# Kernel optimization log

Hardware: AMD Instinct MI355X
Metric: run time of the kernel (lower is better)

Reference implementation:

```python
import jax, jax.numpy as jnp
import numpy as np

HEADS = 8
DIM_HEAD = 64
NH = 16
NW = 16
SCALE = DIM_HEAD ** -0.5


def _avg2x2(a):
    # 2x2 average pool, stride 1, over axes 1,2 of [B,H,W,C] (== unfold+mean in torch)
    return (a[:, :-1, :-1] + a[:, 1:, :-1] + a[:, :-1, 1:] + a[:, 1:, 1:]) * 0.25


def _split_heads(t):
    B, n, _ = t.shape
    return t.reshape(B, n, HEADS, DIM_HEAD).transpose(0, 2, 1, 3)  # b h n d


def setup_inputs() -> dict:
    key = jax.random.key(0)
    ks = jax.random.split(key, 5)
    B, n, dim = 64, 482, 512
    inner = HEADS * DIM_HEAD
    return {
        "x": jax.random.normal(ks[0], (B, n, dim), jnp.float32),
        "mask": jax.random.normal(ks[1], (B, n, dim), jnp.float32),
        "W_qkv": jax.random.normal(ks[2], (3 * inner, dim), jnp.float32) * 0.02,
        "W_out": jax.random.normal(ks[3], (dim, inner), jnp.float32) * 0.02,
        "b_out": jax.random.normal(ks[4], (dim,), jnp.float32) * 0.02,
    }


def reference(x, mask, W_qkv, W_out, b_out):
    sg = jax.lax.stop_gradient
    B, n, dim = x.shape
    inner = HEADS * DIM_HEAD
    nHW = NH * NW            # 256
    nb = (NH - 1) * (NW - 1)  # 225

    # qkv projection
    qkv = x @ W_qkv.T                              # [B,n,3*inner]
    q, k, v = (
        _split_heads(t) for t in jnp.split(qkv, 3, axis=-1)
    )

    # mask path (no grad)
    mask_ = sg(mask)
    updated = (jnp.mean(mask_[:, 1:], axis=-1, keepdims=True) > 0.0).astype(x.dtype)
    updated = jnp.concatenate([jnp.ones_like(updated[:, :1]), updated], axis=1)  # [B,n,1]
    qkv_m = mask_ @ jnp.abs(sg(W_qkv)).T
    q_m, k_m, v_m = (_split_heads(t) for t in jnp.split(qkv_m, 3, axis=-1))
    q_m = q_m / (1e-6 + jnp.max(q_m, axis=2, keepdims=True))
    k_m = k_m / (1e-6 + jnp.max(k_m, axis=2, keepdims=True))
    v_m = v_m / (1e-6 + jnp.max(v_m, axis=2, keepdims=True))
    q_m, k_m, v_m = sg(q_m), sg(k_m), sg(v_m)

    # mask-modulated attention
    dots = jnp.einsum('bhnd,bhmd->bhnm', q * q_m, k * k_m) * SCALE
    attn = jax.nn.softmax(dots, axis=-1)
    out = jnp.einsum('bhnm,bhmd->bhnd', attn, v_m * v)
    out = out.transpose(0, 2, 1, 3).reshape(B, n, inner) * updated

    m = jnp.einsum('bhnm,bhmd->bhnd', sg(attn), v_m)
    m = sg(m.transpose(0, 2, 1, 3).reshape(B, n, inner) * updated)

    # overlap blending (is_overlap=True)
    inv_tail = 1.0 - updated[:, -nb:]
    inv_grid = 1.0 - updated[:, 1:nHW + 1]

    out_bridge = _avg2x2(out[:, 1:nHW + 1].reshape(B, NH, NW, inner)).reshape(B, nb, inner) * inv_tail
    out_origin = jnp.pad(out[:, -nb:].reshape(B, NH - 1, NW - 1, inner),
                         ((0, 0), (1, 1), (1, 1), (0, 0)))
    out_origin = _avg2x2(out_origin).reshape(B, nHW, inner) * inv_grid

    m_bridge = _avg2x2(m[:, 1:nHW + 1].reshape(B, NH, NW, inner)).reshape(B, nb, inner) * inv_tail
    m_origin = jnp.pad(m[:, -nb:].reshape(B, NH - 1, NW - 1, inner),
                       ((0, 0), (1, 1), (1, 1), (0, 0)))
    m_origin = _avg2x2(m_origin).reshape(B, nHW, inner) * inv_grid

    out = out.at[:, 1:nHW + 1].add(out_origin).at[:, -nb:].add(out_bridge)
    m = sg(m.at[:, 1:nHW + 1].add(m_origin).at[:, -nb:].add(m_bridge))

    # nearest-neighbor interpolation of mask means (no grad)
    mm = jnp.mean(m[:, 1:], axis=-1, keepdims=True)          # [B,n-1,1]
    a = mm[:, :nHW].reshape(B, 1, NH, NW)
    inter = jnp.repeat(jnp.repeat(a, 16, axis=2), 16, axis=3)  # [B,1,256,256]
    b = mm[:, -nb:].reshape(B, 1, NH - 1, NW - 1)
    inter_shift = jnp.repeat(jnp.repeat(b, 16, axis=2), 16, axis=3)  # [B,1,240,240]
    inter = inter.at[:, :, 8:-8, 8:-8].set((inter[:, :, 8:-8, 8:-8] + inter_shift) * 0.5)
    inter = sg(inter)

    m = sg(m @ jnp.abs(sg(W_out)).T)

    out_final = out @ W_out.T + b_out
    return out_final, m, inter
```

## Files before the change

### kernel.cpp

```cpp
#include <hip/hip_runtime.h>

#define B_      64
#define NSEQ    482
#define DIM     512
#define HEADS_  8
#define HD      64
#define QKV3    1536
#define NPAD    512
#define MROWS   (B_ * NSEQ)
#define GT      4096

typedef __bf16 v8bf __attribute__((ext_vector_type(8)));
typedef float  v4f  __attribute__((ext_vector_type(4)));
typedef unsigned int v4u __attribute__((ext_vector_type(4)));

typedef __attribute__((address_space(1))) const unsigned short gu16;
typedef __attribute__((address_space(3))) unsigned short lu16;

__device__ __forceinline__ unsigned short f2bf(float f) {
    unsigned u = __float_as_uint(f);
    u += 0x7fffu + ((u >> 16) & 1u);
    return (unsigned short)(u >> 16);
}
__device__ __forceinline__ float bf2f(unsigned short h) {
    return __uint_as_float(((unsigned)h) << 16);
}
__device__ __forceinline__ v8bf vabs8(v8bf x) {
    v4u u;
    __builtin_memcpy(&u, &x, 16);
    u &= (v4u){0x7fff7fffu, 0x7fff7fffu, 0x7fff7fffu, 0x7fff7fffu};
    v8bf r;
    __builtin_memcpy(&r, &u, 16);
    return r;
}

__global__ void k_cvt(const float* __restrict__ s, unsigned short* __restrict__ d, int n4) {
    int i = blockIdx.x * 256 + threadIdx.x;
    if (i < n4) {
        float4 v = ((const float4*)s)[i];
        ushort4 o;
        o.x = f2bf(v.x); o.y = f2bf(v.y); o.z = f2bf(v.z); o.w = f2bf(v.w);
        ((ushort4*)d)[i] = o;
    }
}

__global__ __launch_bounds__(256) void k_cvtmask(const float* __restrict__ mask,
                                                 unsigned short* __restrict__ mb,
                                                 float* __restrict__ upd) {
    int row = blockIdx.x * 4 + (threadIdx.x >> 6);
    int lane = threadIdx.x & 63;
    const float4* p = (const float4*)(mask + (size_t)row * DIM);
    ushort4* d = (ushort4*)(mb + (size_t)row * DIM);
    float s = 0.f;
    #pragma unroll
    for (int j = 0; j < 2; j++) {
        float4 v = p[j * 64 + lane];
        ushort4 o;
        o.x = f2bf(v.x); o.y = f2bf(v.y); o.z = f2bf(v.z); o.w = f2bf(v.w);
        d[j * 64 + lane] = o;
        s += v.x + v.y + v.z + v.w;
    }
    #pragma unroll
    for (int off = 32; off; off >>= 1) s += __shfl_xor(s, off);
    if (lane == 0) {
        int i = row % NSEQ;
        upd[row] = (i == 0) ? 1.f : ((s > 0.f) ? 1.f : 0.f);
    }
}

__global__ __launch_bounds__(512, 4) void k_gemm2(const unsigned short* __restrict__ A1,
                                                  const unsigned short* __restrict__ A2,
                                                  const unsigned short* __restrict__ Bw,
                                                  unsigned short* __restrict__ C1b,
                                                  unsigned short* __restrict__ C2b,
                                                  float* __restrict__ C1f,
                                                  float* __restrict__ C2f,
                                                  const float* __restrict__ bias,
                                                  int N, int K) {
    __shared__ __align__(16) unsigned short As1[3 * GT];
    __shared__ __align__(16) unsigned short As2[3 * GT];
    __shared__ __align__(16) unsigned short Bs[3 * GT];
    int tid = threadIdx.x;
    int lane = tid & 63, w = tid >> 6;
    int grp = w >> 2;
    int wm = (w >> 1) & 1, wn = w & 1;
    int quad = lane >> 4, m16 = lane & 15;

    int nbx = gridDim.x, nwg = nbx * gridDim.y;
    int id = blockIdx.y * nbx + blockIdx.x;
    int q = nwg >> 3, r = nwg & 7;
    int xcd = id & 7, sub = id >> 3;
    int nid = (xcd < r ? xcd * (q + 1) : r * (q + 1) + (xcd - r) * q) + sub;
    int m0 = (nid / nbx) * 128, n0 = (nid % nbx) * 128;

    int srow = tid >> 2, scol = (tid & 3) * 8;
    const unsigned short* gA1 = &A1[(size_t)(m0 + srow) * K + scol];
    const unsigned short* gA2 = &A2[(size_t)(m0 + srow) * K + scol];
    const unsigned short* gB  = &Bw[(size_t)(n0 + srow) * K + scol];
    lu16* lA1 = (lu16*)&As1[w * 512];
    lu16* lA2 = (lu16*)&As2[w * 512];
    lu16* lB  = (lu16*)&Bs[w * 512];

    v4f acc[4][4];
    #pragma unroll
    for (int i = 0; i < 4; i++)
        #pragma unroll
        for (int j = 0; j < 4; j++) acc[i][j] = (v4f){0.f, 0.f, 0.f, 0.f};

    auto STAGE = [&](int bo, int s) {
        int ko = s << 5;
        __builtin_amdgcn_global_load_lds((gu16*)(gA1 + ko), lA1 + bo, 16, 0, 0);
        __builtin_amdgcn_global_load_lds((gu16*)(gA2 + ko), lA2 + bo, 16, 0, 0);
        __builtin_amdgcn_global_load_lds((gu16*)(gB  + ko), lB  + bo, 16, 0, 0);
    };
    const unsigned short* Ams = grp ? As2 : As1;
    auto COMPUTE = [&](int bo) {
        v8bf a[4];
        #pragma unroll
        for (int i = 0; i < 4; i++)
            a[i] = *(const v8bf*)&Ams[bo + (wm * 64 + i * 16 + m16) * 32 + quad * 8];
        #pragma unroll
        for (int j = 0; j < 4; j++) {
            v8bf b = *(const v8bf*)&Bs[bo + (wn * 64 + j * 16 + m16) * 32 + quad * 8];
            if (grp) b = vabs8(b);
            #pragma unroll
            for (int i = 0; i < 4; i++)
                acc[i][j] = __builtin_amdgcn_mfma_f32_16x16x32_bf16(a[i], b, acc[i][j], 0, 0, 0);
        }
    };

    int steps = K >> 5;
    STAGE(0, 0);
    STAGE(GT, 1);
    int b0 = 0, b1 = GT, b2 = 2 * GT;
    for (int s = 0; s < steps; ++s) {
        if (s < steps - 1) asm volatile("s_waitcnt vmcnt(3)" ::: "memory");
        else               asm volatile("s_waitcnt vmcnt(0)" ::: "memory");
        __builtin_amdgcn_s_barrier();
        __builtin_amdgcn_sched_barrier(0);
        if (s + 2 < steps) STAGE(b2, s + 2);
        COMPUTE(b0);
        int t = b0; b0 = b1; b1 = b2; b2 = t;
    }
    __syncthreads();

    if (C1f) {
        float* Cf = grp ? C2f : C1f;
        #pragma unroll
        for (int j = 0; j < 4; j++) {
            int col = n0 + wn * 64 + j * 16 + m16;
            float bi = (bias && !grp) ? bias[col] : 0.f;
            #pragma unroll
            for (int i = 0; i < 4; i++) {
                int rowb = m0 + wm * 64 + i * 16 + quad * 4;
                #pragma unroll
                for (int r = 0; r < 4; r++) {
                    size_t off = (size_t)(rowb + r) * N + col;
                    Cf[off] = acc[i][j][r] + bi;
                }
            }
        }
    } else {
        unsigned short* Cb = grp ? C2b : C1b;
        unsigned short* wbuf = &As1[w * 1024];
        int rr = lane >> 2;
        int c0 = ((lane & 3) * 2) ^ ((rr >> 1) & 7);
        size_t colb = n0 + wn * 64 + (lane & 3) * 16;
        #pragma unroll
        for (int i = 0; i < 4; i++) {
            #pragma unroll
            for (int j = 0; j < 4; j++)
                #pragma unroll
                for (int r = 0; r < 4; r++) {
                    int row = quad * 4 + r;
                    int e = j * 16 + m16;
                    int es = ((((e >> 3) ^ ((row >> 1) & 7)) << 3) | (e & 7));
                    wbuf[row * 64 + es] = f2bf(acc[i][j][r]);
                }
            int4 p0 = *(const int4*)&wbuf[rr * 64 + c0 * 8];
            int4 p1 = *(const int4*)&wbuf[rr * 64 + (c0 ^ 1) * 8];
            size_t off0 = (size_t)(m0 + wm * 64 + i * 16 + rr) * N + colb;
            *(int4*)&Cb[off0] = p0;
            *(int4*)&Cb[off0 + 8] = p1;
        }
    }
}

__global__ void k_colmax(const unsigned short* __restrict__ qm, float* __restrict__ invsc) {
    int b = blockIdx.x;
    int c = blockIdx.y * 256 + threadIdx.x;
    const unsigned short* p = qm + (size_t)b * NSEQ * QKV3 + c;
    float mx = -1e30f;
    for (int i = 0; i < NSEQ; i++) mx = fmaxf(mx, bf2f(p[(size_t)i * QKV3]));
    invsc[b * QKV3 + c] = 1.f / (1e-6f + mx);
}

__global__ __launch_bounds__(256) void k_build(const unsigned short* __restrict__ qkv,
                                               const unsigned short* __restrict__ qm,
                                               const float* __restrict__ invsc,
                                               unsigned short* __restrict__ QQ,
                                               unsigned short* __restrict__ KK,
                                               unsigned short* __restrict__ VVt,
                                               unsigned short* __restrict__ VMt) {
    __shared__ unsigned short tv[64][72];
    __shared__ unsigned short tm[64][72];
    int tid = threadIdx.x;
    int dd = tid & 63, il = tid >> 6;
    int it = blockIdx.x, h = blockIdx.y, b = blockIdx.z;
    int i0 = it * 64;
    size_t bh = (size_t)(b * HEADS_ + h);
    int c = h * HD + dd;
    float invq = invsc[b * QKV3 + c] * 0.125f;
    float invk = invsc[b * QKV3 + 512 + c];
    float invv = invsc[b * QKV3 + 1024 + c];
    #pragma unroll 4
    for (int p = 0; p < 16; p++) {
        int li = p * 4 + il;
        int i = i0 + li;
        unsigned short oq = 0, ok = 0, ov = 0, om = 0;
        if (i < NSEQ) {
            size_t base = ((size_t)(b * NSEQ + i)) * QKV3 + c;
            float q  = bf2f(qkv[base]),        qv = bf2f(qm[base]);
            float kk = bf2f(qkv[base + 512]),  kv = bf2f(qm[base + 512]);
            float vv = bf2f(qkv[base + 1024]), vm = bf2f(qm[base + 1024]);
            oq = f2bf(q * qv * invq);
            ok = f2bf(kk * kv * invk);
            float vmn = vm * invv;
            ov = f2bf(vv * vmn);
            om = f2bf(vmn);
        }
        QQ[(bh * NPAD + i) * HD + dd] = oq;
        KK[(bh * NPAD + i) * HD + dd] = ok;
        tv[li][dd] = ov;
        tm[li][dd] = om;
    }
    __syncthreads();
    #pragma unroll 4
    for (int p = 0; p < 16; p++) {
        int dr = p * 4 + il;
        VVt[(bh * HD + dr) * NPAD + i0 + dd] = tv[dd][dr];
        VMt[(bh * HD + dr) * NPAD + i0 + dd] = tm[dd][dr];
    }
}

__global__ __launch_bounds__(256, 3) void k_attn(const unsigned short* __restrict__ QQ,
                                                 const unsigned short* __restrict__ KK,
                                                 const unsigned short* __restrict__ VVt,
                                                 const unsigned short* __restrict__ VMt,
                                                 const float* __restrict__ upd,
                                                 float* __restrict__ OUT1,
                                                 float* __restrict__ M1) {
    __shared__ __align__(16) unsigned short Ks[2][32 * 72];
    __shared__ __align__(16) unsigned short Vs[2][64 * 40];
    __shared__ __align__(16) unsigned short Ms[2][64 * 40];
    __shared__ __align__(16) unsigned short Ps[4][32 * 40];

    int tid = threadIdx.x;
    int w = tid >> 6, lane = tid & 63;
    int quad = lane >> 4, m16 = lane & 15;
    int id = (blockIdx.z * 8 + blockIdx.y) * 4 + blockIdx.x;
    int nid = (id & 7) * 256 + (id >> 3);
    int b = nid >> 5, h = (nid >> 2) & 7;
    int q0 = (nid & 3) * 128 + w * 32;
    size_t bh = (size_t)(b * HEADS_ + h);

    v8bf aq[2][2];
    #pragma unroll
    for (int s = 0; s < 2; s++) {
        const unsigned short* qb = &QQ[(bh * NPAD + q0 + s * 16 + m16) * HD];
        aq[s][0] = *(const v8bf*)&qb[quad * 8];
        aq[s][1] = *(const v8bf*)&qb[32 + quad * 8];
    }

    v4f vacc[2][4], macc[2][4];
    #pragma unroll
    for (int s = 0; s < 2; s++)
        #pragma unroll
        for (int dt = 0; dt < 4; dt++) {
            vacc[s][dt] = (v4f){0.f, 0.f, 0.f, 0.f};
            macc[s][dt] = (v4f){0.f, 0.f, 0.f, 0.f};
        }
    float lrun[2][4];
    #pragma unroll
    for (int s = 0; s < 2; s++)
        #pragma unroll
        for (int r = 0; r < 4; r++) lrun[s][r] = 0.f;

    const unsigned short* gK = &KK[bh * NPAD * HD + tid * 8];
    const unsigned short* gV = &VVt[(bh * HD + (tid >> 2)) * NPAD + (tid & 3) * 8];
    const unsigned short* gM = &VMt[(bh * HD + (tid >> 2)) * NPAD + (tid & 3) * 8];
    int oK = (tid >> 3) * 72 + (tid & 7) * 8;
    int oV = (tid >> 2) * 40 + (tid & 3) * 8;
    unsigned short* Pw = &Ps[w][0];

    int4 rk = *(const int4*)gK;
    int4 rv = *(const int4*)gV;
    int4 rm = *(const int4*)gM;

    for (int ic = 0; ic < 16; ++ic) {
        int buf = ic & 1;
        *(int4*)&Ks[buf][oK] = rk;
        *(int4*)&Vs[buf][oV] = rv;
        *(int4*)&Ms[buf][oV] = rm;
        if (ic < 15) {
            rk = *(const int4*)(gK + (ic + 1) * 32 * HD);
            rv = *(const int4*)(gV + (ic + 1) * 32);
            rm = *(const int4*)(gM + (ic + 1) * 32);
        }
        __syncthreads();

        v8bf kf[2][2];
        #pragma unroll
        for (int t = 0; t < 2; t++) {
            kf[t][0] = *(const v8bf*)&Ks[buf][(t * 16 + m16) * 72 + quad * 8];
            kf[t][1] = *(const v8bf*)&Ks[buf][(t * 16 + m16) * 72 + 32 + quad * 8];
        }
        v4f S[2][2];
        #pragma unroll
        for (int s = 0; s < 2; s++)
            #pragma unroll
            for (int t = 0; t < 2; t++) {
                v4f a = (v4f){0.f, 0.f, 0.f, 0.f};
                a = __builtin_amdgcn_mfma_f32_16x16x32_bf16(aq[s][0], kf[t][0], a, 0, 0, 0);
                a = __builtin_amdgcn_mfma_f32_16x16x32_bf16(aq[s][1], kf[t][1], a, 0, 0, 0);
                S[s][t] = a;
            }

        int i0 = ic * 32;
        if (i0 + 32 > NSEQ) {
            bool x0 = (i0 + m16) >= NSEQ;
            bool x1 = (i0 + 16 + m16) >= NSEQ;
            #pragma unroll
            for (int s = 0; s < 2; s++)
                #pragma unroll
                for (int r = 0; r < 4; r++) {
                    if (x0) S[s][0][r] = -1e30f;
                    if (x1) S[s][1][r] = -1e30f;
                }
        }

        #pragma unroll
        for (int s = 0; s < 2; s++)
            #pragma unroll
            for (int r = 0; r < 4; r++) {
                float e0 = __expf(S[s][0][r]);
                float e1 = __expf(S[s][1][r]);
                lrun[s][r] += e0 + e1;
                Pw[(s * 16 + quad * 4 + r) * 40 + m16] = f2bf(e0);
                Pw[(s * 16 + quad * 4 + r) * 40 + 16 + m16] = f2bf(e1);
            }

        v8bf ap[2];
        ap[0] = *(const v8bf*)&Pw[m16 * 40 + quad * 8];
        ap[1] = *(const v8bf*)&Pw[(16 + m16) * 40 + quad * 8];

        #pragma unroll
        for (int dt = 0; dt < 4; dt++) {
            v8bf bv = *(const v8bf*)&Vs[buf][(dt * 16 + m16) * 40 + quad * 8];
            v8bf bm = *(const v8bf*)&Ms[buf][(dt * 16 + m16) * 40 + quad * 8];
            #pragma unroll
            for (int s = 0; s < 2; s++) {
                vacc[s][dt] = __builtin_amdgcn_mfma_f32_16x16x32_bf16(ap[s], bv, vacc[s][dt], 0, 0, 0);
                macc[s][dt] = __builtin_amdgcn_mfma_f32_16x16x32_bf16(ap[s], bm, macc[s][dt], 0, 0, 0);
            }
        }
    }

    #pragma unroll
    for (int s = 0; s < 2; s++)
        #pragma unroll
        for (int r = 0; r < 4; r++) {
            float sum = lrun[s][r];
            sum += __shfl_xor(sum, 1);
            sum += __shfl_xor(sum, 2);
            sum += __shfl_xor(sum, 4);
            sum += __shfl_xor(sum, 8);
            float iv = 1.f / sum;
            int iq = q0 + s * 16 + quad * 4 + r;
            if (iq < NSEQ) {
                float u = upd[b * NSEQ + iq] * iv;
                size_t off = ((size_t)(b * NSEQ + iq)) * DIM + h * HD + m16;
                #pragma unroll
                for (int dt = 0; dt < 4; dt++) {
                    OUT1[off + dt * 16] = vacc[s][dt][r] * u;
                    M1[off + dt * 16]   = macc[s][dt][r] * u;
                }
            }
        }
}

__global__ __launch_bounds__(256) void k_blend(const float* __restrict__ O1,
                                               const float* __restrict__ Mm,
                                               const float* __restrict__ upd,
                                               unsigned short* __restrict__ O2,
                                               unsigned short* __restrict__ M2,
                                               float* __restrict__ mm) {
    int blk = blockIdx.x;
    int b = blk / NSEQ, i = blk - b * NSEQ;
    int tid = threadIdx.x;
    size_t rb = (size_t)blk * DIM;
    int ns = 0;
    size_t src[4];
    float wgt = 0.f;
    if (i >= 1) {
        wgt = 0.25f * (1.f - upd[blk]);
        if (wgt != 0.f) {
            if (i <= 256) {
                int g = i - 1, gy = g >> 4, gx = g & 15;
                #pragma unroll
                for (int dy = 0; dy < 2; dy++)
                    #pragma unroll
                    for (int dx = 0; dx < 2; dx++) {
                        int sy = gy - 1 + dy, sx = gx - 1 + dx;
                        if (sy >= 0 && sy < 15 && sx >= 0 && sx < 15)
                            src[ns++] = ((size_t)(b * NSEQ + 257 + sy * 15 + sx)) * DIM;
                    }
            } else {
                int t = i - 257, ty = t / 15, tx = t - ty * 15;
                #pragma unroll
                for (int dy = 0; dy < 2; dy++)
                    #pragma unroll
                    for (int dx = 0; dx < 2; dx++)
                        src[ns++] = ((size_t)(b * NSEQ + 1 + (ty + dy) * 16 + (tx + dx))) * DIM;
            }
        }
    }
    float msum = 0.f;
    for (int c = tid; c < DIM; c += 256) {
        float o = O1[rb + c], m = Mm[rb + c];
        float ao = 0.f, am = 0.f;
        for (int s = 0; s < ns; s++) { ao += O1[src[s] + c]; am += Mm[src[s] + c]; }
        o += wgt * ao;
        m += wgt * am;
        O2[rb + c] = f2bf(o);
        M2[rb + c] = f2bf(m);
        msum += m;
    }
    #pragma unroll
    for (int off = 32; off; off >>= 1) msum += __shfl_xor(msum, off);
    __shared__ float red[4];
    if ((tid & 63) == 0) red[tid >> 6] = msum;
    __syncthreads();
    if (tid == 0 && i >= 1)
        mm[b * 481 + i - 1] = (red[0] + red[1] + red[2] + red[3]) * (1.f / 512.f);
}

__global__ void k_inter(const float* __restrict__ mm, float* __restrict__ dst) {
    int idx = blockIdx.x * 256 + threadIdx.x;
    int b = idx >> 16, rem = idx & 65535;
    int y = rem >> 8, x = rem & 255;
    const float* mb = mm + b * 481;
    float v = mb[((y >> 4) << 4) + (x >> 4)];
    if (y >= 8 && y < 248 && x >= 8 && x < 248)
        v = 0.5f * (v + mb[256 + ((y - 8) >> 4) * 15 + ((x - 8) >> 4)]);
    dst[idx] = v;
}

extern "C" void kernel_launch(void* const* d_in, const int* in_sizes, int n_in,
                              void* d_out, int out_size, void* d_ws, size_t ws_size,
                              hipStream_t stream) {
    const float* x    = (const float*)d_in[0];
    const float* mask = (const float*)d_in[1];
    const float* Wqkv = (const float*)d_in[2];
    const float* Wout = (const float*)d_in[3];
    const float* bout = (const float*)d_in[4];
    float* out = (float*)d_out;

    char* ws = (char*)d_ws;
    size_t o = 0;
    auto alloc = [&](size_t bytes) -> char* {
        char* r = ws + o;
        o += (bytes + 255) & ~(size_t)255;
        return r;
    };
    unsigned short* xb    = (unsigned short*)alloc((size_t)MROWS * DIM * 2);
    unsigned short* maskb = (unsigned short*)alloc((size_t)MROWS * DIM * 2);
    unsigned short* Wb    = (unsigned short*)alloc((size_t)QKV3 * DIM * 2);
    unsigned short* Wob   = (unsigned short*)alloc((size_t)DIM * DIM * 2);
    unsigned short* qkvb  = (unsigned short*)alloc((size_t)MROWS * QKV3 * 2);
    unsigned short* qkvmb = (unsigned short*)alloc((size_t)MROWS * QKV3 * 2);
    float* upd  = (float*)alloc((size_t)MROWS * 4);
    float* invs = (float*)alloc((size_t)B_ * QKV3 * 4);
    float* mm   = (float*)alloc((size_t)B_ * 481 * 4);
    unsigned short* QQ  = (unsigned short*)alloc((size_t)B_ * HEADS_ * NPAD * HD * 2);
    unsigned short* KK  = (unsigned short*)alloc((size_t)B_ * HEADS_ * NPAD * HD * 2);
    unsigned short* VVt = (unsigned short*)alloc((size_t)B_ * HEADS_ * NPAD * HD * 2);
    unsigned short* VMt = (unsigned short*)alloc((size_t)B_ * HEADS_ * NPAD * HD * 2);
    float* OUT1 = (float*)qkvb;
    float* M1p  = (float*)qkvmb;
    unsigned short* O2 = xb;
    unsigned short* M2 = maskb;

    k_cvt<<<(MROWS * DIM / 4) / 256, 256, 0, stream>>>(x, xb, MROWS * DIM / 4);
    k_cvtmask<<<MROWS / 4, 256, 0, stream>>>(mask, maskb, upd);
    k_cvt<<<(QKV3 * DIM / 4) / 256, 256, 0, stream>>>(Wqkv, Wb, QKV3 * DIM / 4);
    k_cvt<<<(DIM * DIM / 4) / 256, 256, 0, stream>>>(Wout, Wob, DIM * DIM / 4);

    dim3 g1(QKV3 / 128, MROWS / 128);
    k_gemm2<<<g1, 512, 0, stream>>>(xb, maskb, Wb, qkvb, qkvmb,
                                    nullptr, nullptr, nullptr, QKV3, DIM);

    k_colmax<<<dim3(B_, QKV3 / 256), 256, 0, stream>>>(qkvmb, invs);
    k_build<<<dim3(8, HEADS_, B_), 256, 0, stream>>>(qkvb, qkvmb, invs, QQ, KK, VVt, VMt);

    k_attn<<<dim3(4, HEADS_, B_), 256, 0, stream>>>(QQ, KK, VVt, VMt, upd, OUT1, M1p);

    k_blend<<<MROWS, 256, 0, stream>>>(OUT1, M1p, upd, O2, M2, mm);
    k_inter<<<(B_ * 65536) / 256, 256, 0, stream>>>(mm, out + (size_t)2 * MROWS * DIM);

    dim3 g2(DIM / 128, MROWS / 128);
    k_gemm2<<<g2, 512, 0, stream>>>(O2, M2, Wob, nullptr, nullptr,
                                    out, out + (size_t)MROWS * DIM, bout, DIM, DIM);
}
```

Baseline: 757.7 us.

## Fuse column-max into QKV GEMM epilogue, widen GEMM K-tile, add MFMA priority hints

Several ideas are combined. The mask GEMM epilogue now reduces per-batch column maxima of the fp32 accumulators and records them with order-preserving atomicMax. A tiny kernel then converts those maxima to reciprocal scales, replacing the separate column-max pass that re-read the bf16 qkv_m tensor. The GEMM switches from 3-stage K=32 tiles to double-buffered K=64 tiles with an XOR-swizzled LDS layout and a lower occupancy bound. s_setprio hints are also added around the MFMA sections in both the GEMM and the attention kernel. The trade-offs are atomic contention, max taken on fp32 rather than bf16-rounded values, and less load/compute overlap from the shallower pipeline.

```diff
diff --git a/kernel.cpp b/kernel.cpp
--- a/kernel.cpp
+++ b/kernel.cpp
@@ -8,7 +8,7 @@
 #define QKV3    1536
 #define NPAD    512
 #define MROWS   (B_ * NSEQ)
-#define GT      4096
+#define GT      8192
 
 typedef __bf16 v8bf __attribute__((ext_vector_type(8)));
 typedef float  v4f  __attribute__((ext_vector_type(4)));
@@ -32,6 +32,10 @@
     v8bf r;
     __builtin_memcpy(&r, &u, 16);
     return r;
+}
+__device__ __forceinline__ unsigned f2o(float f) {
+    unsigned b = __float_as_uint(f);
+    return (b & 0x80000000u) ? ~b : (b | 0x80000000u);
 }
 
 __global__ void k_cvt(const float* __restrict__ s, unsigned short* __restrict__ d, int n4) {
@@ -68,7 +72,7 @@
     }
 }
 
-__global__ __launch_bounds__(512, 4) void k_gemm2(const unsigned short* __restrict__ A1,
+__global__ __launch_bounds__(512, 2) void k_gemm2(const unsigned short* __restrict__ A1,
                                                   const unsigned short* __restrict__ A2,
                                                   const unsigned short* __restrict__ Bw,
                                                   unsigned short* __restrict__ C1b,
@@ -76,14 +80,16 @@
                                                   float* __restrict__ C1f,
                                                   float* __restrict__ C2f,
                                                   const float* __restrict__ bias,
+                                                  unsigned* __restrict__ cm,
                                                   int N, int K) {
-    __shared__ __align__(16) unsigned short As1[3 * GT];
-    __shared__ __align__(16) unsigned short As2[3 * GT];
-    __shared__ __align__(16) unsigned short Bs[3 * GT];
+    __shared__ __align__(16) unsigned short As1[2 * GT];
+    __shared__ __align__(16) unsigned short As2[2 * GT];
+    __shared__ __align__(16) unsigned short Bs[2 * GT];
     int tid = threadIdx.x;
     int lane = tid & 63, w = tid >> 6;
     int grp = w >> 2;
-    int wm = (w >> 1) & 1, wn = w & 1;
+    int ws = w & 3;
+    int wm = ws >> 1, wn = ws & 1;
     int quad = lane >> 4, m16 = lane & 15;
 
     int nbx = gridDim.x, nwg = nbx * gridDim.y;
@@ -93,10 +99,12 @@
     int nid = (xcd < r ? xcd * (q + 1) : r * (q + 1) + (xcd - r) * q) + sub;
     int m0 = (nid / nbx) * 128, n0 = (nid % nbx) * 128;
 
-    int srow = tid >> 2, scol = (tid & 3) * 8;
+    int srow = w * 8 + (lane >> 3);
+    int scol = (((lane & 7) ^ (lane >> 3)) & 7) * 8;
     const unsigned short* gA1 = &A1[(size_t)(m0 + srow) * K + scol];
     const unsigned short* gA2 = &A2[(size_t)(m0 + srow) * K + scol];
     const unsigned short* gB  = &Bw[(size_t)(n0 + srow) * K + scol];
+    size_t rK = (size_t)64 * K;
     lu16* lA1 = (lu16*)&As1[w * 512];
     lu16* lA2 = (lu16*)&As2[w * 512];
     lu16* lB  = (lu16*)&Bs[w * 512];
@@ -108,41 +116,81 @@
         for (int j = 0; j < 4; j++) acc[i][j] = (v4f){0.f, 0.f, 0.f, 0.f};
 
     auto STAGE = [&](int bo, int s) {
-        int ko = s << 5;
+        size_t ko = (size_t)(s << 6);
         __builtin_amdgcn_global_load_lds((gu16*)(gA1 + ko), lA1 + bo, 16, 0, 0);
+        __builtin_amdgcn_global_load_lds((gu16*)(gA1 + rK + ko), lA1 + bo + 4096, 16, 0, 0);
         __builtin_amdgcn_global_load_lds((gu16*)(gA2 + ko), lA2 + bo, 16, 0, 0);
-        __builtin_amdgcn_global_load_lds((gu16*)(gB  + ko), lB  + bo, 16, 0, 0);
+        __builtin_amdgcn_global_load_lds((gu16*)(gA2 + rK + ko), lA2 + bo + 4096, 16, 0, 0);
+        __builtin_amdgcn_global_load_lds((gu16*)(gB + ko), lB + bo, 16, 0, 0);
+        __builtin_amdgcn_global_load_lds((gu16*)(gB + rK + ko), lB + bo + 4096, 16, 0, 0);
     };
     const unsigned short* Ams = grp ? As2 : As1;
     auto COMPUTE = [&](int bo) {
-        v8bf a[4];
+        v8bf a[4][2], bfr[2];
         #pragma unroll
         for (int i = 0; i < 4; i++)
-            a[i] = *(const v8bf*)&Ams[bo + (wm * 64 + i * 16 + m16) * 32 + quad * 8];
+            #pragma unroll
+            for (int k2 = 0; k2 < 2; k2++)
+                a[i][k2] = *(const v8bf*)&Ams[bo + (wm * 64 + i * 16 + m16) * 64
+                                              + (((k2 * 4 + quad) ^ (m16 & 7)) * 8)];
         #pragma unroll
         for (int j = 0; j < 4; j++) {
-            v8bf b = *(const v8bf*)&Bs[bo + (wn * 64 + j * 16 + m16) * 32 + quad * 8];
-            if (grp) b = vabs8(b);
-            #pragma unroll
-            for (int i = 0; i < 4; i++)
-                acc[i][j] = __builtin_amdgcn_mfma_f32_16x16x32_bf16(a[i], b, acc[i][j], 0, 0, 0);
+            #pragma unroll
+            for (int k2 = 0; k2 < 2; k2++) {
+                v8bf b = *(const v8bf*)&Bs[bo + (wn * 64 + j * 16 + m16) * 64
+                                           + (((k2 * 4 + quad) ^ (m16 & 7)) * 8)];
+                bfr[k2] = grp ? vabs8(b) : b;
+            }
+            #pragma unroll
+            for (int i = 0; i < 4; i++) {
+                acc[i][j] = __builtin_amdgcn_mfma_f32_16x16x32_bf16(a[i][0], bfr[0], acc[i][j], 0, 0, 0);
+                acc[i][j] = __builtin_amdgcn_mfma_f32_16x16x32_bf16(a[i][1], bfr[1], acc[i][j], 0, 0, 0);
+            }
         }
     };
 
-    int steps = K >> 5;
+    int steps = K >> 6;
     STAGE(0, 0);
-    STAGE(GT, 1);
-    int b0 = 0, b1 = GT, b2 = 2 * GT;
     for (int s = 0; s < steps; ++s) {
-        if (s < steps - 1) asm volatile("s_waitcnt vmcnt(3)" ::: "memory");
-        else               asm volatile("s_waitcnt vmcnt(0)" ::: "memory");
+        int bo = (s & 1) * GT;
+        asm volatile("s_waitcnt vmcnt(0)" ::: "memory");
         __builtin_amdgcn_s_barrier();
         __builtin_amdgcn_sched_barrier(0);
-        if (s + 2 < steps) STAGE(b2, s + 2);
-        COMPUTE(b0);
-        int t = b0; b0 = b1; b1 = b2; b2 = t;
+        if (s + 1 < steps) STAGE(bo ^ GT, s + 1);
+        __builtin_amdgcn_s_setprio(1);
+        COMPUTE(bo);
+        __builtin_amdgcn_s_setprio(0);
     }
     __syncthreads();
+
+    if (cm && grp) {
+        int bb0 = (m0 + wm * 64) / NSEQ;
+        int bound = (bb0 + 1) * NSEQ;
+        int rbase = m0 + wm * 64;
+        bool spill = (bound < rbase + 64);
+        #pragma unroll
+        for (int j = 0; j < 4; j++) {
+            float mx0 = -1e30f, mx1 = -1e30f;
+            #pragma unroll
+            for (int i = 0; i < 4; i++)
+                #pragma unroll
+                for (int rr = 0; rr < 4; rr++) {
+                    int row = rbase + i * 16 + quad * 4 + rr;
+                    float v = acc[i][j][rr];
+                    if (row < bound) mx0 = fmaxf(mx0, v);
+                    else             mx1 = fmaxf(mx1, v);
+                }
+            mx0 = fmaxf(mx0, __shfl_xor(mx0, 16));
+            mx0 = fmaxf(mx0, __shfl_xor(mx0, 32));
+            mx1 = fmaxf(mx1, __shfl_xor(mx1, 16));
+            mx1 = fmaxf(mx1, __shfl_xor(mx1, 32));
+            if (quad == 0) {
+                int col = n0 + wn * 64 + j * 16 + m16;
+                atomicMax(&cm[bb0 * N + col], f2o(mx0));
+                if (spill) atomicMax(&cm[(bb0 + 1) * N + col], f2o(mx1));
+            }
+        }
+    }
 
     if (C1f) {
         float* Cf = grp ? C2f : C1f;
@@ -154,9 +202,9 @@
             for (int i = 0; i < 4; i++) {
                 int rowb = m0 + wm * 64 + i * 16 + quad * 4;
                 #pragma unroll
-                for (int r = 0; r < 4; r++) {
-                    size_t off = (size_t)(rowb + r) * N + col;
-                    Cf[off] = acc[i][j][r] + bi;
+                for (int r2 = 0; r2 < 4; r2++) {
+                    size_t off = (size_t)(rowb + r2) * N + col;
+                    Cf[off] = acc[i][j][r2] + bi;
                 }
             }
         }
@@ -171,11 +219,11 @@
             #pragma unroll
             for (int j = 0; j < 4; j++)
                 #pragma unroll
-                for (int r = 0; r < 4; r++) {
-                    int row = quad * 4 + r;
+                for (int r2 = 0; r2 < 4; r2++) {
+                    int row = quad * 4 + r2;
                     int e = j * 16 + m16;
                     int es = ((((e >> 3) ^ ((row >> 1) & 7)) << 3) | (e & 7));
-                    wbuf[row * 64 + es] = f2bf(acc[i][j][r]);
+                    wbuf[row * 64 + es] = f2bf(acc[i][j][r2]);
                 }
             int4 p0 = *(const int4*)&wbuf[rr * 64 + c0 * 8];
             int4 p1 = *(const int4*)&wbuf[rr * 64 + (c0 ^ 1) * 8];
@@ -186,13 +234,13 @@
     }
 }
 
-__global__ void k_colmax(const unsigned short* __restrict__ qm, float* __restrict__ invsc) {
-    int b = blockIdx.x;
-    int c = blockIdx.y * 256 + threadIdx.x;
-    const unsigned short* p = qm + (size_t)b * NSEQ * QKV3 + c;
-    float mx = -1e30f;
-    for (int i = 0; i < NSEQ; i++) mx = fmaxf(mx, bf2f(p[(size_t)i * QKV3]));
-    invsc[b * QKV3 + c] = 1.f / (1e-6f + mx);
+__global__ void k_invs(float* __restrict__ p, int n) {
+    int i = blockIdx.x * 256 + threadIdx.x;
+    if (i < n) {
+        unsigned u = ((const unsigned*)p)[i];
+        unsigned b = (u & 0x80000000u) ? (u & 0x7fffffffu) : ~u;
+        p[i] = 1.f / (1e-6f + __uint_as_float(b));
+    }
 }
 
 __global__ __launch_bounds__(256) void k_build(const unsigned short* __restrict__ qkv,
@@ -316,6 +364,7 @@
             kf[t][1] = *(const v8bf*)&Ks[buf][(t * 16 + m16) * 72 + 32 + quad * 8];
         }
         v4f S[2][2];
+        __builtin_amdgcn_s_setprio(1);
         #pragma unroll
         for (int s = 0; s < 2; s++)
             #pragma unroll
@@ -325,6 +374,7 @@
                 a = __builtin_amdgcn_mfma_f32_16x16x32_bf16(aq[s][1], kf[t][1], a, 0, 0, 0);
                 S[s][t] = a;
             }
+        __builtin_amdgcn_s_setprio(0);
 
         int i0 = ic * 32;
         if (i0 + 32 > NSEQ) {
@@ -354,6 +404,7 @@
         ap[0] = *(const v8bf*)&Pw[m16 * 40 + quad * 8];
         ap[1] = *(const v8bf*)&Pw[(16 + m16) * 40 + quad * 8];
 
+        __builtin_amdgcn_s_setprio(1);
         #pragma unroll
         for (int dt = 0; dt < 4; dt++) {
             v8bf bv = *(const v8bf*)&Vs[buf][(dt * 16 + m16) * 40 + quad * 8];
@@ -364,6 +415,7 @@
                 macc[s][dt] = __builtin_amdgcn_mfma_f32_16x16x32_bf16(ap[s], bm, macc[s][dt], 0, 0, 0);
             }
         }
+        __builtin_amdgcn_s_setprio(0);
     }
 
     #pragma unroll
@@ -495,12 +547,14 @@
     k_cvtmask<<<MROWS / 4, 256, 0, stream>>>(mask, maskb, upd);
     k_cvt<<<(QKV3 * DIM / 4) / 256, 256, 0, stream>>>(Wqkv, Wb, QKV3 * DIM / 4);
     k_cvt<<<(DIM * DIM / 4) / 256, 256, 0, stream>>>(Wout, Wob, DIM * DIM / 4);
+    hipMemsetAsync(invs, 0, (size_t)B_ * QKV3 * 4, stream);
 
     dim3 g1(QKV3 / 128, MROWS / 128);
     k_gemm2<<<g1, 512, 0, stream>>>(xb, maskb, Wb, qkvb, qkvmb,
-                                    nullptr, nullptr, nullptr, QKV3, DIM);
-
-    k_colmax<<<dim3(B_, QKV3 / 256), 256, 0, stream>>>(qkvmb, invs);
+                                    nullptr, nullptr, nullptr, (unsigned*)invs,
+                                    QKV3, DIM);
+
+    k_invs<<<(B_ * QKV3) / 256, 256, 0, stream>>>(invs, B_ * QKV3);
     k_build<<<dim3(8, HEADS_, B_), 256, 0, stream>>>(qkvb, qkvmb, invs, QQ, KK, VVt, VMt);
 
     k_attn<<<dim3(4, HEADS_, B_), 256, 0, stream>>>(QQ, KK, VVt, VMt, upd, OUT1, M1p);
@@ -510,5 +564,6 @@
 
     dim3 g2(DIM / 128, MROWS / 128);
     k_gemm2<<<g2, 512, 0, stream>>>(O2, M2, Wob, nullptr, nullptr,
-                                    out, out + (size_t)MROWS * DIM, bout, DIM, DIM);
-}
+                                    out, out + (size_t)MROWS * DIM, bout, nullptr,
+                                    DIM, DIM);
+}
```

Result: faster. 727.0 us (-4.0%).
